# Optimization experiments

Hardware: AMD Instinct MI355X
Metric: run time of the kernel (lower is better)

## Reference

```python
import jax, jax.numpy as jnp
import numpy as np

B, N, F_IN = 8, 1024, 128
H, F_OUT = 4, 64
NEG_INF = -9e15


def setup_inputs() -> dict:
    key = jax.random.key(0)
    k1, k2, k3, k4 = jax.random.split(key, 4)
    x = jax.random.normal(k1, (B, N, F_IN), dtype=jnp.float32)
    adj = jax.random.randint(k2, (B, N, N), 0, 2, dtype=jnp.int32)
    W = jax.random.normal(k3, (F_IN, H * F_OUT), dtype=jnp.float32) * 0.05
    a = jax.random.normal(k4, (H, 2 * F_OUT), dtype=jnp.float32)
    return {"x": x, "adj": adj, "W": W, "a": a}


def reference(x, adj, W, a):
    # x: [B,N,F_in], adj: [B,N,N], W: [F_in, H*F_out], a: [H, 2*F_out]
    Bs, Ns, _ = x.shape
    Hh = a.shape[0]
    Fo = a.shape[1] // 2
    h = (x @ W).reshape(Bs, Ns, Hh, Fo)            # [B,N,H,F]
    # e_{bnmh} = a . cat(h_i, h_j) = a_src . h_n + a_dst . h_m  (no O(N^2) concat)
    a_src, a_dst = a[:, :Fo], a[:, Fo:]
    e_src = jnp.einsum('bnhf,hf->bnh', h, a_src)    # [B,N,H]
    e_dst = jnp.einsum('bmhf,hf->bmh', h, a_dst)    # [B,N,H]
    e = e_src[:, :, None, :] + e_dst[:, None, :, :]  # [B,N,N,H]
    e = jax.nn.leaky_relu(e, negative_slope=0.2)
    e = jnp.where(adj[..., None] > 0, e, NEG_INF)
    attention = jax.nn.softmax(e, axis=2)           # softmax over neighbors m
    h_prime = jnp.einsum('bnmh,bmhf->bnhf', attention, h)
    return h_prime.mean(axis=2)                     # [B,N,F_out]
```

## Files before the change

kernel.cpp:

```cpp
#include <hip/hip_runtime.h>
#include <math.h>

#define Bsz 8
#define Nsz 1024
#define FIN 128
#define Hh  4
#define FO  64
#define COLS 256
#define TN  16
#define TM  32
#define BN  (Bsz*Nsz)
#define SHIFT 12.0f

typedef __attribute__((ext_vector_type(8))) short short8;
typedef __attribute__((ext_vector_type(4))) float f32x4;

static __device__ inline ushort f2bf(float f) {
    uint u = __float_as_uint(f);
    u += 0x7FFFu + ((u >> 16) & 1u);
    return (ushort)(u >> 16);
}
static __device__ inline float bf2f(ushort h) { return __uint_as_float(((uint)h) << 16); }

__global__ __launch_bounds__(256) void gat_proj(
    const float* __restrict__ x, const float* __restrict__ W,
    const float* __restrict__ a, ushort* __restrict__ h_gB,
    float* __restrict__ es_g, float* __restrict__ ed_g)
{
    __shared__ float x_lds[16 * FIN];
    const int j   = threadIdx.x;
    const int blk = blockIdx.x;
    const int b   = blk >> 6;
    const int n0  = (blk & 63) * 16;
    const long rowb = (long)b * Nsz + n0;

    const float4* xg4 = (const float4*)(x + rowb * FIN);
    float4* xl4 = (float4*)x_lds;
    xl4[j]       = xg4[j];
    xl4[j + 256] = xg4[j + 256];
    __syncthreads();

    float hv[16];
    #pragma unroll
    for (int r = 0; r < 16; r++) hv[r] = 0.f;

    const float* Wc = W + j;
    for (int k4 = 0; k4 < FIN / 4; k4++) {
        float w0 = Wc[(k4*4 + 0) * COLS];
        float w1 = Wc[(k4*4 + 1) * COLS];
        float w2 = Wc[(k4*4 + 2) * COLS];
        float w3 = Wc[(k4*4 + 3) * COLS];
        #pragma unroll
        for (int r = 0; r < 16; r++) {
            float4 xv = xl4[r * (FIN/4) + k4];
            hv[r] = fmaf(xv.x, w0, fmaf(xv.y, w1, fmaf(xv.z, w2, fmaf(xv.w, w3, hv[r]))));
        }
    }

    {
        const int mt = n0 >> 5, kin0 = n0 & 31;
        union { ushort u[16]; int4 v4[2]; } pk;
        #pragma unroll
        for (int r = 0; r < 16; r++) pk.u[r] = f2bf(hv[r]);
        int4* dst = (int4*)(h_gB + (((long)(b*32 + mt) * 256 + j) * 32 + kin0));
        dst[0] = pk.v4[0]; dst[1] = pk.v4[1];
    }

    const int w = j >> 6, f = j & 63;
    const float as = a[w * (2*FO) + f];
    const float ad = a[w * (2*FO) + FO + f];
    #pragma unroll
    for (int r = 0; r < 16; r++) {
        float s1 = hv[r] * as;
        float s2 = hv[r] * ad;
        #pragma unroll
        for (int off = 32; off > 0; off >>= 1) {
            s1 += __shfl_xor(s1, off, 64);
            s2 += __shfl_xor(s2, off, 64);
        }
        if (f == 0) {
            es_g[(long)w * BN + rowb + r] = s1;
            ed_g[(long)w * BN + rowb + r] = s2;
        }
    }
}

__global__ __launch_bounds__(256, 4) void gat_attn(
    const int* __restrict__ adj, const ushort* __restrict__ h_gB,
    const float* __restrict__ es_g, const float* __restrict__ ed_g,
    float* __restrict__ out)
{
    __shared__ ushort hT[TM * COLS];
    __shared__ ushort p_bf[TN * Hh * TM];
    __shared__ float  l_lds[TN * Hh];

    const int j    = threadIdx.x;
    const int w    = j >> 6;
    const int lane = j & 63;
    const int quad = lane >> 4;
    const int n16  = lane & 15;
    const int mi   = lane & 31;
    const int hh   = lane >> 5;
    const int b    = blockIdx.y;
    const int n0   = blockIdx.x * TN;
    const long rowb = (long)b * Nsz + n0;

    float es[4][2];
    #pragma unroll
    for (int r4 = 0; r4 < 4; r4++)
        #pragma unroll
        for (int ii = 0; ii < 2; ii++)
            es[r4][ii] = es_g[(long)(hh*2 + ii) * BN + rowb + w*4 + r4];

    f32x4 acc[4];
    #pragma unroll
    for (int c4 = 0; c4 < 4; c4++)
        #pragma unroll
        for (int r = 0; r < 4; r++) acc[c4][r] = 0.f;

    float l_part[4][2];
    #pragma unroll
    for (int r4 = 0; r4 < 4; r4++) { l_part[r4][0] = 0.f; l_part[r4][1] = 0.f; }

    short8 hreg[4]; int areg[4]; float edreg[2];
    const short8* hb8 = (const short8*)h_gB;
    #define PREFETCH(t)                                                             \
        {                                                                           \
            const short8* g = hb8 + (long)(b*32 + (t)) * 1024;                      \
            hreg[0] = g[j]; hreg[1] = g[j+256]; hreg[2] = g[j+512]; hreg[3] = g[j+768]; \
            const int m0p = (t) * TM;                                               \
            _Pragma("unroll")                                                       \
            for (int r4 = 0; r4 < 4; r4++)                                          \
                areg[r4] = adj[(rowb + w*4 + r4) * (long)Nsz + m0p + mi];           \
            _Pragma("unroll")                                                       \
            for (int ii = 0; ii < 2; ii++)                                          \
                edreg[ii] = ed_g[(long)(hh*2 + ii) * BN + (long)b * Nsz + m0p + mi];\
        }
    PREFETCH(0);

    short8* hT8 = (short8*)hT;

    for (int t = 0; t < Nsz / TM; t++) {
        hT8[j] = hreg[0]; hT8[j+256] = hreg[1]; hT8[j+512] = hreg[2]; hT8[j+768] = hreg[3];
        __syncthreads();

        int a_c[4]; float ed_c[2];
        #pragma unroll
        for (int r4 = 0; r4 < 4; r4++) a_c[r4] = areg[r4];
        ed_c[0] = edreg[0]; ed_c[1] = edreg[1];
        if (t + 1 < Nsz / TM) PREFETCH(t + 1);

        #pragma unroll
        for (int r4 = 0; r4 < 4; r4++) {
            const int r = w*4 + r4;
            #pragma unroll
            for (int ii = 0; ii < 2; ii++) {
                const int hx = hh*2 + ii;
                float s = es[r4][ii] + ed_c[ii];
                s = s > 0.f ? s : 0.2f * s;
                float p = (a_c[r4] > 0) ? __expf(s - SHIFT) : 0.f;
                ushort pb = f2bf(p);
                p_bf[(r * Hh + hx) * TM + mi] = pb;
                l_part[r4][ii] += bf2f(pb);
            }
        }
        __syncthreads();

        {
            const short8* pb8 = (const short8*)p_bf;
            short8 af = pb8[(n16 * Hh + w) * 4 + quad];
            #pragma unroll
            for (int c4 = 0; c4 < 4; c4++) {
                short8 bfrag = hT8[(w*64 + c4*16 + n16) * 4 + quad];
                acc[c4] = __builtin_amdgcn_mfma_f32_16x16x32_bf16(af, bfrag, acc[c4], 0, 0, 0);
            }
        }
        __syncthreads();
    }

    #pragma unroll
    for (int r4 = 0; r4 < 4; r4++)
        #pragma unroll
        for (int ii = 0; ii < 2; ii++) {
            float lp = l_part[r4][ii];
            #pragma unroll
            for (int off = 1; off < 32; off <<= 1) lp += __shfl_xor(lp, off, 64);
            if (mi == 0) l_lds[(w*4 + r4) * Hh + hh*2 + ii] = lp;
        }
    __syncthreads();

    float* o_lds = (float*)hT;
    float rinv[4];
    #pragma unroll
    for (int reg = 0; reg < 4; reg++) {
        const int row = quad*4 + reg;
        rinv[reg] = 0.25f / l_lds[row * Hh + w];
    }
    #pragma unroll
    for (int c4 = 0; c4 < 4; c4++)
        #pragma unroll
        for (int reg = 0; reg < 4; reg++) {
            const int row = quad*4 + reg;
            o_lds[(w * TN + row) * FO + c4*16 + n16] = acc[c4][reg] * rinv[reg];
        }
    __syncthreads();

    {
        const int f2 = j & 63, rb = j >> 6;
        #pragma unroll
        for (int i = 0; i < 4; i++) {
            const int r = i*4 + rb;
            const float sum = o_lds[(0*TN + r)*FO + f2] + o_lds[(1*TN + r)*FO + f2]
                            + o_lds[(2*TN + r)*FO + f2] + o_lds[(3*TN + r)*FO + f2];
            out[(rowb + r) * FO + f2] = sum;
        }
    }
}

extern "C" void kernel_launch(void* const* d_in, const int* in_sizes, int n_in,
                              void* d_out, int out_size, void* d_ws, size_t ws_size,
                              hipStream_t stream) {
    const float* x   = (const float*)d_in[0];
    const int*   adj = (const int*)d_in[1];
    const float* W   = (const float*)d_in[2];
    const float* a   = (const float*)d_in[3];
    float* out = (float*)d_out;

    ushort* h_gB = (ushort*)d_ws;
    float*  es_g = (float*)((char*)d_ws + (size_t)BN * COLS * sizeof(ushort));
    float*  ed_g = es_g + (size_t)Hh * BN;

    gat_proj<<<dim3(Bsz * Nsz / 16), dim3(256), 0, stream>>>(x, W, a, h_gB, es_g, ed_g);
    gat_attn<<<dim3(Nsz / TN, Bsz), dim3(256), 0, stream>>>(adj, h_gB, es_g, ed_g, out);
}
```

Measured before the change: 134.5 us.

## Use MFMA for projection, double-buffer attention LDS with padded strides

Adds a prep kernel that transposes W to bf16 and rewrites the projection to use bf16 MFMA instead of scalar FP32 FMAs, computing the e_src/e_dst dot products from the MFMA accumulators. The attention kernel now double-buffers the h and p tiles in LDS with padded strides to avoid bank conflicts. This leaves one barrier per iteration, so the score computation for the next tile overlaps the MFMAs on the current one. Occupancy is lowered to 3 blocks per SM because of the larger LDS footprint, and the projection now rounds x and W to bf16, which adds precision loss.

```diff
diff --git a/kernel.cpp b/kernel.cpp
--- a/kernel.cpp
+++ b/kernel.cpp
@@ -11,6 +11,9 @@
 #define TM  32
 #define BN  (Bsz*Nsz)
 #define SHIFT 12.0f
+#define HSTR 40
+#define PSTR 136
+#define XSTR 136
 
 typedef __attribute__((ext_vector_type(8))) short short8;
 typedef __attribute__((ext_vector_type(4))) float f32x4;
@@ -22,85 +25,111 @@
 }
 static __device__ inline float bf2f(ushort h) { return __uint_as_float(((uint)h) << 16); }
 
+__global__ __launch_bounds__(256) void gat_prep(const float* __restrict__ W,
+                                                ushort* __restrict__ Wt)
+{
+    const int g = blockIdx.x * 256 + threadIdx.x;
+    const int n = g >> 3, kc = (g & 7) * 16;
+    ushort u[16];
+    #pragma unroll
+    for (int i = 0; i < 16; i++) u[i] = f2bf(W[(kc + i) * COLS + n]);
+    int4* dst = (int4*)(Wt + n * FIN + kc);
+    dst[0] = ((int4*)u)[0];
+    dst[1] = ((int4*)u)[1];
+}
+
 __global__ __launch_bounds__(256) void gat_proj(
-    const float* __restrict__ x, const float* __restrict__ W,
+    const float* __restrict__ x, const ushort* __restrict__ Wt,
     const float* __restrict__ a, ushort* __restrict__ h_gB,
     float* __restrict__ es_g, float* __restrict__ ed_g)
 {
-    __shared__ float x_lds[16 * FIN];
-    const int j   = threadIdx.x;
-    const int blk = blockIdx.x;
-    const int b   = blk >> 6;
-    const int n0  = (blk & 63) * 16;
-    const long rowb = (long)b * Nsz + n0;
-
-    const float4* xg4 = (const float4*)(x + rowb * FIN);
-    float4* xl4 = (float4*)x_lds;
-    xl4[j]       = xg4[j];
-    xl4[j + 256] = xg4[j + 256];
-    __syncthreads();
-
-    float hv[16];
-    #pragma unroll
-    for (int r = 0; r < 16; r++) hv[r] = 0.f;
-
-    const float* Wc = W + j;
-    for (int k4 = 0; k4 < FIN / 4; k4++) {
-        float w0 = Wc[(k4*4 + 0) * COLS];
-        float w1 = Wc[(k4*4 + 1) * COLS];
-        float w2 = Wc[(k4*4 + 2) * COLS];
-        float w3 = Wc[(k4*4 + 3) * COLS];
-        #pragma unroll
-        for (int r = 0; r < 16; r++) {
-            float4 xv = xl4[r * (FIN/4) + k4];
-            hv[r] = fmaf(xv.x, w0, fmaf(xv.y, w1, fmaf(xv.z, w2, fmaf(xv.w, w3, hv[r]))));
-        }
-    }
+    __shared__ ushort xs[16 * XSTR];
+    const int j    = threadIdx.x;
+    const int w    = j >> 6, lane = j & 63, quad = lane >> 4, n16 = lane & 15;
+    const int b    = blockIdx.x >> 6, mt16 = blockIdx.x & 63;
+    const long rowbase = (long)b * Nsz + mt16 * 16;
+
+    short8 bfr[4][4];
+    #pragma unroll
+    for (int kk = 0; kk < 4; kk++)
+        #pragma unroll
+        for (int c4 = 0; c4 < 4; c4++)
+            bfr[kk][c4] = *(const short8*)(Wt + (w*64 + c4*16 + n16) * FIN + kk*32 + quad*8);
 
     {
-        const int mt = n0 >> 5, kin0 = n0 & 31;
-        union { ushort u[16]; int4 v4[2]; } pk;
-        #pragma unroll
-        for (int r = 0; r < 16; r++) pk.u[r] = f2bf(hv[r]);
-        int4* dst = (int4*)(h_gB + (((long)(b*32 + mt) * 256 + j) * 32 + kin0));
-        dst[0] = pk.v4[0]; dst[1] = pk.v4[1];
-    }
-
-    const int w = j >> 6, f = j & 63;
-    const float as = a[w * (2*FO) + f];
-    const float ad = a[w * (2*FO) + FO + f];
-    #pragma unroll
-    for (int r = 0; r < 16; r++) {
-        float s1 = hv[r] * as;
-        float s2 = hv[r] * ad;
-        #pragma unroll
-        for (int off = 32; off > 0; off >>= 1) {
-            s1 += __shfl_xor(s1, off, 64);
-            s2 += __shfl_xor(s2, off, 64);
-        }
-        if (f == 0) {
-            es_g[(long)w * BN + rowb + r] = s1;
-            ed_g[(long)w * BN + rowb + r] = s2;
-        }
-    }
-}
-
-__global__ __launch_bounds__(256, 4) void gat_attn(
+        const int r = j >> 4, k0 = (j & 15) * 8;
+        const float4* g4 = (const float4*)(x + (rowbase + r) * FIN + k0);
+        float4 v0 = g4[0], v1 = g4[1];
+        ushort u[8] = { f2bf(v0.x), f2bf(v0.y), f2bf(v0.z), f2bf(v0.w),
+                        f2bf(v1.x), f2bf(v1.y), f2bf(v1.z), f2bf(v1.w) };
+        *(int4*)(xs + r * XSTR + k0) = *(int4*)u;
+    }
+    __syncthreads();
+
+    f32x4 acc[4];
+    #pragma unroll
+    for (int c4 = 0; c4 < 4; c4++)
+        #pragma unroll
+        for (int r = 0; r < 4; r++) acc[c4][r] = 0.f;
+
+    #pragma unroll
+    for (int kk = 0; kk < 4; kk++) {
+        short8 af = *(const short8*)(xs + n16 * XSTR + kk*32 + quad*8);
+        #pragma unroll
+        for (int c4 = 0; c4 < 4; c4++)
+            acc[c4] = __builtin_amdgcn_mfma_f32_16x16x32_bf16(af, bfr[kk][c4], acc[c4], 0, 0, 0);
+    }
+
+    const int mtile = mt16 >> 1;
+    const int kbase = (mt16 & 1) * 16 + quad * 4;
+    #pragma unroll
+    for (int c4 = 0; c4 < 4; c4++) {
+        uint2 pk;
+        pk.x = (uint)f2bf(acc[c4][0]) | ((uint)f2bf(acc[c4][1]) << 16);
+        pk.y = (uint)f2bf(acc[c4][2]) | ((uint)f2bf(acc[c4][3]) << 16);
+        const int c = w*64 + c4*16 + n16;
+        *(uint2*)(h_gB + (((long)(b*32 + mtile) * COLS + c) * 32 + kbase)) = pk;
+    }
+
+    float aS[4], aD[4];
+    #pragma unroll
+    for (int c4 = 0; c4 < 4; c4++) {
+        aS[c4] = a[w * (2*FO) + c4*16 + n16];
+        aD[c4] = a[w * (2*FO) + FO + c4*16 + n16];
+    }
+    #pragma unroll
+    for (int reg = 0; reg < 4; reg++) {
+        float ps = 0.f, pd = 0.f;
+        #pragma unroll
+        for (int c4 = 0; c4 < 4; c4++) {
+            ps = fmaf(acc[c4][reg], aS[c4], ps);
+            pd = fmaf(acc[c4][reg], aD[c4], pd);
+        }
+        #pragma unroll
+        for (int off = 1; off < 16; off <<= 1) {
+            ps += __shfl_xor(ps, off, 64);
+            pd += __shfl_xor(pd, off, 64);
+        }
+        if (n16 == 0) {
+            const long row = rowbase + quad*4 + reg;
+            es_g[(long)w * BN + row] = ps;
+            ed_g[(long)w * BN + row] = pd;
+        }
+    }
+}
+
+__global__ __launch_bounds__(256, 3) void gat_attn(
     const int* __restrict__ adj, const ushort* __restrict__ h_gB,
     const float* __restrict__ es_g, const float* __restrict__ ed_g,
     float* __restrict__ out)
 {
-    __shared__ ushort hT[TM * COLS];
-    __shared__ ushort p_bf[TN * Hh * TM];
+    __shared__ ushort hT[2][COLS * HSTR];
+    __shared__ ushort pT[2][TN * PSTR];
     __shared__ float  l_lds[TN * Hh];
 
     const int j    = threadIdx.x;
-    const int w    = j >> 6;
-    const int lane = j & 63;
-    const int quad = lane >> 4;
-    const int n16  = lane & 15;
-    const int mi   = lane & 31;
-    const int hh   = lane >> 5;
+    const int w    = j >> 6, lane = j & 63, quad = lane >> 4, n16 = lane & 15;
+    const int mi   = lane & 31, hh = lane >> 5;
     const int b    = blockIdx.y;
     const int n0   = blockIdx.x * TN;
     const long rowb = (long)b * Nsz + n0;
@@ -124,57 +153,56 @@
 
     short8 hreg[4]; int areg[4]; float edreg[2];
     const short8* hb8 = (const short8*)h_gB;
-    #define PREFETCH(t)                                                             \
-        {                                                                           \
-            const short8* g = hb8 + (long)(b*32 + (t)) * 1024;                      \
-            hreg[0] = g[j]; hreg[1] = g[j+256]; hreg[2] = g[j+512]; hreg[3] = g[j+768]; \
-            const int m0p = (t) * TM;                                               \
-            _Pragma("unroll")                                                       \
-            for (int r4 = 0; r4 < 4; r4++)                                          \
-                areg[r4] = adj[(rowb + w*4 + r4) * (long)Nsz + m0p + mi];           \
-            _Pragma("unroll")                                                       \
-            for (int ii = 0; ii < 2; ii++)                                          \
-                edreg[ii] = ed_g[(long)(hh*2 + ii) * BN + (long)b * Nsz + m0p + mi];\
-        }
+
+#define PREFETCH(t) {                                                           \
+    const short8* g = hb8 + (long)(b*32 + (t)) * 1024;                          \
+    hreg[0] = g[j]; hreg[1] = g[j+256]; hreg[2] = g[j+512]; hreg[3] = g[j+768]; \
+    const int m0p = (t) * TM;                                                   \
+    _Pragma("unroll")                                                           \
+    for (int r4 = 0; r4 < 4; r4++)                                              \
+        areg[r4] = adj[(rowb + w*4 + r4) * (long)Nsz + m0p + mi];               \
+    _Pragma("unroll")                                                           \
+    for (int ii = 0; ii < 2; ii++)                                              \
+        edreg[ii] = ed_g[(long)(hh*2 + ii) * BN + (long)b * Nsz + m0p + mi]; }
+
+#define STAGE(buf) {                                                            \
+    _Pragma("unroll")                                                           \
+    for (int i = 0; i < 4; i++) {                                               \
+        const int s = j + 256*i;                                                \
+        *(short8*)(&hT[buf][(s >> 2) * HSTR + (s & 3) * 8]) = hreg[i]; } }
+
+#define PHASE_S(buf) {                                                          \
+    _Pragma("unroll")                                                           \
+    for (int r4 = 0; r4 < 4; r4++) {                                            \
+        _Pragma("unroll")                                                       \
+        for (int ii = 0; ii < 2; ii++) {                                        \
+            float s = es[r4][ii] + edreg[ii];                                   \
+            s = fmaxf(s, 0.2f * s);                                             \
+            float p = (areg[r4] > 0) ? __expf(s - SHIFT) : 0.f;                 \
+            ushort pb = f2bf(p);                                                \
+            pT[buf][(w*4 + r4) * PSTR + (hh*2 + ii) * TM + mi] = pb;            \
+            l_part[r4][ii] += bf2f(pb); } } }
+
+#define PHASE_A(buf) {                                                          \
+    short8 af = *(const short8*)(&pT[buf][n16 * PSTR + w * TM + quad * 8]);     \
+    _Pragma("unroll")                                                           \
+    for (int c4 = 0; c4 < 4; c4++) {                                            \
+        short8 bfv = *(const short8*)(&hT[buf][(w*64 + c4*16 + n16) * HSTR + quad * 8]); \
+        acc[c4] = __builtin_amdgcn_mfma_f32_16x16x32_bf16(af, bfv, acc[c4], 0, 0, 0); } }
+
     PREFETCH(0);
-
-    short8* hT8 = (short8*)hT;
+    STAGE(0); PHASE_S(0);
+    PREFETCH(1);
+    __syncthreads();
 
     for (int t = 0; t < Nsz / TM; t++) {
-        hT8[j] = hreg[0]; hT8[j+256] = hreg[1]; hT8[j+512] = hreg[2]; hT8[j+768] = hreg[3];
-        __syncthreads();
-
-        int a_c[4]; float ed_c[2];
-        #pragma unroll
-        for (int r4 = 0; r4 < 4; r4++) a_c[r4] = areg[r4];
-        ed_c[0] = edreg[0]; ed_c[1] = edreg[1];
-        if (t + 1 < Nsz / TM) PREFETCH(t + 1);
-
-        #pragma unroll
-        for (int r4 = 0; r4 < 4; r4++) {
-            const int r = w*4 + r4;
-            #pragma unroll
-            for (int ii = 0; ii < 2; ii++) {
-                const int hx = hh*2 + ii;
-                float s = es[r4][ii] + ed_c[ii];
-                s = s > 0.f ? s : 0.2f * s;
-                float p = (a_c[r4] > 0) ? __expf(s - SHIFT) : 0.f;
-                ushort pb = f2bf(p);
-                p_bf[(r * Hh + hx) * TM + mi] = pb;
-                l_part[r4][ii] += bf2f(pb);
-            }
-        }
-        __syncthreads();
-
-        {
-            const short8* pb8 = (const short8*)p_bf;
-            short8 af = pb8[(n16 * Hh + w) * 4 + quad];
-            #pragma unroll
-            for (int c4 = 0; c4 < 4; c4++) {
-                short8 bfrag = hT8[(w*64 + c4*16 + n16) * 4 + quad];
-                acc[c4] = __builtin_amdgcn_mfma_f32_16x16x32_bf16(af, bfrag, acc[c4], 0, 0, 0);
-            }
-        }
+        const int cur = t & 1;
+        if (t < Nsz / TM - 1) {
+            STAGE(cur ^ 1);
+            PHASE_S(cur ^ 1);
+            if (t < Nsz / TM - 2) PREFETCH(t + 2);
+        }
+        PHASE_A(cur);
         __syncthreads();
     }
 
@@ -189,20 +217,16 @@
         }
     __syncthreads();
 
-    float* o_lds = (float*)hT;
+    float* o_lds = (float*)&hT[0][0];
     float rinv[4];
     #pragma unroll
-    for (int reg = 0; reg < 4; reg++) {
-        const int row = quad*4 + reg;
-        rinv[reg] = 0.25f / l_lds[row * Hh + w];
-    }
+    for (int reg = 0; reg < 4; reg++)
+        rinv[reg] = 0.25f / l_lds[(quad*4 + reg) * Hh + w];
     #pragma unroll
     for (int c4 = 0; c4 < 4; c4++)
         #pragma unroll
-        for (int reg = 0; reg < 4; reg++) {
-            const int row = quad*4 + reg;
-            o_lds[(w * TN + row) * FO + c4*16 + n16] = acc[c4][reg] * rinv[reg];
-        }
+        for (int reg = 0; reg < 4; reg++)
+            o_lds[(w * TN + quad*4 + reg) * FO + c4*16 + n16] = acc[c4][reg] * rinv[reg];
     __syncthreads();
 
     {
@@ -215,6 +239,10 @@
             out[(rowb + r) * FO + f2] = sum;
         }
     }
+#undef PREFETCH
+#undef STAGE
+#undef PHASE_S
+#undef PHASE_A
 }
 
 extern "C" void kernel_launch(void* const* d_in, const int* in_sizes, int n_in,
@@ -226,10 +254,12 @@
     const float* a   = (const float*)d_in[3];
     float* out = (float*)d_out;
 
-    ushort* h_gB = (ushort*)d_ws;
-    float*  es_g = (float*)((char*)d_ws + (size_t)BN * COLS * sizeof(ushort));
+    ushort* Wt   = (ushort*)d_ws;
+    ushort* h_gB = Wt + (size_t)COLS * FIN;
+    float*  es_g = (float*)(h_gB + (size_t)BN * COLS);
     float*  ed_g = es_g + (size_t)Hh * BN;
 
-    gat_proj<<<dim3(Bsz * Nsz / 16), dim3(256), 0, stream>>>(x, W, a, h_gB, es_g, ed_g);
-    gat_attn<<<dim3(Nsz / TN, Bsz), dim3(256), 0, stream>>>(adj, h_gB, es_g, ed_g, out);
-}
+    gat_prep<<<dim3(8),            dim3(256), 0, stream>>>(W, Wt);
+    gat_proj<<<dim3(Bsz*Nsz/16),   dim3(256), 0, stream>>>(x, Wt, a, h_gB, es_g, ed_g);
+    gat_attn<<<dim3(Nsz/TN, Bsz),  dim3(256), 0, stream>>>(adj, h_gB, es_g, ed_g, out);
+}
```

Result: faster. 114.5 us (-14.9%).
